# Kernel optimization log

Hardware: AMD Instinct MI355X
Metric: run time of the kernel (lower is better)

Reference implementation:

```python
import jax, jax.numpy as jnp
import numpy as np
from jax import lax

B, T, E, D = 32, 4096, 512, 512     # batch, x_steps, eunits, dunits
A, C, F = 128, 32, 15               # attn_dim, conv_channel, aconv_filts
K = 2 * F + 1                       # location conv kernel size
NEG = -1e9


def setup_inputs() -> dict:
    key = jax.random.key(0)
    ks = jax.random.split(key, 12)
    value = jax.random.normal(ks[0], (B, T, E), dtype=jnp.float32)
    value_length = jax.random.randint(ks[1], (B,), T // 2, T + 1).astype(jnp.int32)
    query = jax.random.normal(ks[2], (B, D), dtype=jnp.float32)
    # dirac initialization per initialize_weights()
    prev_attn_weight = jax.nn.one_hot(jnp.zeros((B,), jnp.int32), T, dtype=jnp.float32)
    accum_attn_weight = prev_attn_weight
    s = 0.02
    Wv = jax.random.normal(ks[3], (E, A), dtype=jnp.float32) * s
    bv = jnp.zeros((A,), jnp.float32)
    Wq = jax.random.normal(ks[4], (D, A), dtype=jnp.float32) * s
    conv_k = jax.random.normal(ks[5], (K, 1, C), dtype=jnp.float32) * s  # WIO
    Wl = jax.random.normal(ks[6], (C, A), dtype=jnp.float32) * s
    att_v = jax.random.normal(ks[7], (A,), dtype=jnp.float32)
    att_g = jnp.asarray(np.sqrt(1.0 / A), jnp.float32)
    att_b = jnp.zeros((A,), jnp.float32)
    score_bias = jnp.asarray(0.0, jnp.float32)
    return {"value": value, "value_length": value_length, "query": query,
            "accum_attn_weight": accum_attn_weight, "prev_attn_weight": prev_attn_weight,
            "Wv": Wv, "bv": bv, "Wq": Wq, "conv_k": conv_k, "Wl": Wl,
            "att_v": att_v, "att_g": att_g, "att_b": att_b, "score_bias": score_bias}


def _forward(value, value_length, query, accum_attn_weight, prev_attn_weight,
             Wv, bv, Wq, conv_k, Wl, att_v, att_g, att_b, score_bias):
    # projections
    densed_value = value @ Wv + bv                      # [B,T,A]
    densed_query = (query @ Wq)[:, None, :]             # [B,1,A]
    # location conv over accumulated weights, channels_last SAME
    loc = lax.conv_general_dilated(accum_attn_weight[:, :, None], conv_k,
                                   window_strides=(1,), padding='SAME',
                                   dimension_numbers=('NWC', 'WIO', 'NWC'))  # [B,T,C]
    attn_location = loc @ Wl                            # [B,T,A]
    # weight-normalized energy
    normed_v = att_g * att_v * lax.rsqrt(jnp.sum(jnp.square(att_v)))
    x = attn_location + densed_value + densed_query
    energy = jnp.einsum('bta,a->bt', jnp.tanh(x + att_b), normed_v) + score_bias
    mask = jnp.arange(T)[None, :] < value_length[:, None]
    energy = energy + (1.0 - mask.astype(energy.dtype)) * NEG
    # soft stepwise monotonic update (training=False: no sigmoid noise)
    p = jax.nn.sigmoid(energy)                          # [B,T]
    shifted = jnp.concatenate(
        [jnp.zeros((value.shape[0], 1), p.dtype),
         prev_attn_weight[:, :-1] * (1.0 - p[:, :-1])], axis=1)
    attn_weight = prev_attn_weight * p + shifted        # [B,T]
    attn_c = jnp.einsum('bt,bte->be', attn_weight, value)
    return attn_c, attn_weight


def reference(value, value_length, query, accum_attn_weight, prev_attn_weight,
              Wv, bv, Wq, conv_k, Wl, att_v, att_g, att_b, score_bias):
    return _forward(value, value_length, query, accum_attn_weight, prev_attn_weight,
                    Wv, bv, Wq, conv_k, Wl, att_v, att_g, att_b, score_bias)
```

## Files before the change

### kernel.cpp

```cpp
#include <hip/hip_runtime.h>
#include <hip/hip_bf16.h>

#define TT 4096
#define EE 512
#define AA 128

typedef short short8 __attribute__((ext_vector_type(8)));
typedef float f32x4 __attribute__((ext_vector_type(4)));

__device__ __forceinline__ short f2bf(float f) {
    union { float f; unsigned u; } v; v.f = f;
    unsigned r = v.u + 0x7fffu + ((v.u >> 16) & 1u);
    return (short)(r >> 16);
}

#define WS_WVT   0
#define WS_QBIAS 139264
#define WS_NV    155648
#define WS_P     156160
#define WS_PART  680448

__global__ void prep_wvt(const float* __restrict__ Wv, const float* __restrict__ conv_k,
                         const float* __restrict__ Wl, short* __restrict__ wvt) {
    int idx = blockIdx.x * 256 + threadIdx.x;
    int a = idx / 544, k = idx % 544;
    float val = 0.f;
    if (k < 512) {
        val = Wv[k * 128 + a];
    } else if (k < 543) {
        int kk = k - 512;
        float s = 0.f;
        #pragma unroll
        for (int c = 0; c < 32; ++c) s += conv_k[kk * 32 + c] * Wl[c * 128 + a];
        val = s;
    }
    wvt[a * 544 + k] = f2bf(val);
}

__global__ void prep_qbias(const float* __restrict__ query, const float* __restrict__ Wq,
                           const float* __restrict__ bv, const float* __restrict__ att_b,
                           const float* __restrict__ att_v, const float* __restrict__ att_g,
                           float* __restrict__ q_bias, float* __restrict__ nv) {
    int b = blockIdx.x, a = threadIdx.x;
    float s = 0.f;
    for (int d = 0; d < 512; ++d) s += query[b * 512 + d] * Wq[d * 128 + a];
    q_bias[b * 128 + a] = s + bv[a] + att_b[a];
    if (b == 0) {
        float ss = 0.f;
        for (int i = 0; i < 128; ++i) { float t = att_v[i]; ss += t * t; }
        nv[a] = att_g[0] * att_v[a] * rsqrtf(ss);
    }
}

__global__ __launch_bounds__(256) void energy_kernel(
    const float* __restrict__ value, const int* __restrict__ vlen,
    const float* __restrict__ accum, const short* __restrict__ wvt,
    const float* __restrict__ q_bias, const float* __restrict__ nv,
    const float* __restrict__ score_bias, float* __restrict__ p_buf) {

    __shared__ __align__(16) short As[64 * 40];
    __shared__ __align__(16) short Bs[128 * 40];

    int bid = blockIdx.x;
    int b  = bid >> 6;
    int t0 = (bid & 63) << 6;
    int tid = threadIdx.x;
    int l = tid & 63, w = tid >> 6;
    int l15 = l & 15, g = l >> 4;

    f32x4 acc[8];
    #pragma unroll
    for (int i = 0; i < 8; ++i) acc[i] = (f32x4){0.f, 0.f, 0.f, 0.f};

    int ar = tid >> 2;
    int ac = (tid & 3) * 8;
    int br = tid >> 1;
    int bc = (tid & 1) * 16;

    const float* aglob = value + ((size_t)(b * TT + t0 + ar)) * EE;

    for (int kc = 0; kc < 17; ++kc) {
        {
            const short* src = wvt + br * 544 + kc * 32 + bc;
            short8 s0 = *(const short8*)(src);
            short8 s1 = *(const short8*)(src + 8);
            *(short8*)(&Bs[br * 40 + bc])     = s0;
            *(short8*)(&Bs[br * 40 + bc + 8]) = s1;
        }
        if (kc < 16) {
            const float4* src = (const float4*)(aglob + kc * 32 + ac);
            float4 v0 = src[0], v1 = src[1];
            short8 h;
            h[0] = f2bf(v0.x); h[1] = f2bf(v0.y); h[2] = f2bf(v0.z); h[3] = f2bf(v0.w);
            h[4] = f2bf(v1.x); h[5] = f2bf(v1.y); h[6] = f2bf(v1.z); h[7] = f2bf(v1.w);
            *(short8*)(&As[ar * 40 + ac]) = h;
        } else {
            short8 h;
            #pragma unroll
            for (int i = 0; i < 8; ++i) {
                int kk = ac + i;
                int t = t0 + ar - 15 + kk;
                float v = (kk < 31 && t >= 0 && t < TT) ? accum[b * TT + t] : 0.f;
                h[i] = f2bf(v);
            }
            *(short8*)(&As[ar * 40 + ac]) = h;
        }
        __syncthreads();

        short8 af = *(const short8*)(&As[(w * 16 + l15) * 40 + g * 8]);
        #pragma unroll
        for (int t8 = 0; t8 < 8; ++t8) {
            short8 bf = *(const short8*)(&Bs[(t8 * 16 + l15) * 40 + g * 8]);
            acc[t8] = __builtin_amdgcn_mfma_f32_16x16x32_bf16(af, bf, acc[t8], 0, 0, 0);
        }
        __syncthreads();
    }

    float qb[8], nvv[8];
    #pragma unroll
    for (int t8 = 0; t8 < 8; ++t8) {
        int a = t8 * 16 + l15;
        qb[t8]  = q_bias[b * 128 + a];
        nvv[t8] = nv[a];
    }
    int len = vlen[b];
    float sb = score_bias[0];
    #pragma unroll
    for (int j = 0; j < 4; ++j) {
        float e = 0.f;
        #pragma unroll
        for (int t8 = 0; t8 < 8; ++t8)
            e += tanhf(acc[t8][j] + qb[t8]) * nvv[t8];
        e += __shfl_xor(e, 1);
        e += __shfl_xor(e, 2);
        e += __shfl_xor(e, 4);
        e += __shfl_xor(e, 8);
        if (l15 == 0) {
            int t = t0 + w * 16 + g * 4 + j;
            float p = 0.f;
            if (t < len) { float ee = e + sb; p = 1.f / (1.f + expf(-ee)); }
            p_buf[b * TT + t] = p;
        }
    }
}

__global__ void weight_kernel(const float* __restrict__ p_buf, const float* __restrict__ prev,
                              float* __restrict__ outw) {
    int i = blockIdx.x * 256 + threadIdx.x;
    int t = i & (TT - 1);
    float w = prev[i] * p_buf[i];
    if (t > 0) w += prev[i - 1] * (1.f - p_buf[i - 1]);
    outw[i] = w;
}

__global__ __launch_bounds__(256) void ctx_partial(const float* __restrict__ value,
                                                   const float* __restrict__ wbuf,
                                                   float* __restrict__ part) {
    __shared__ float wsm[512];
    int b = blockIdx.x, tc = blockIdx.y;
    int tid = threadIdx.x;
    wsm[tid]       = wbuf[b * TT + tc * 512 + tid];
    wsm[tid + 256] = wbuf[b * TT + tc * 512 + tid + 256];
    __syncthreads();
    float ax = 0.f, ay = 0.f;
    const float* vbase = value + ((size_t)b * TT + tc * 512) * EE + tid * 2;
    for (int tt = 0; tt < 512; ++tt) {
        float wv = wsm[tt];
        if (wv != 0.f) {
            float2 v = *(const float2*)(vbase + (size_t)tt * EE);
            ax += wv * v.x; ay += wv * v.y;
        }
    }
    float2 r; r.x = ax; r.y = ay;
    *(float2*)(part + ((b * 8 + tc) * 512) + tid * 2) = r;
}

__global__ void ctx_reduce(const float* __restrict__ part, float* __restrict__ outc) {
    int idx = blockIdx.x * 256 + threadIdx.x;
    int b = idx >> 9, e = idx & 511;
    float s = 0.f;
    #pragma unroll
    for (int tc = 0; tc < 8; ++tc) s += part[(b * 8 + tc) * 512 + e];
    outc[idx] = s;
}

extern "C" void kernel_launch(void* const* d_in, const int* in_sizes, int n_in,
                              void* d_out, int out_size, void* d_ws, size_t ws_size,
                              hipStream_t stream) {
    const float* value  = (const float*)d_in[0];
    const int*   vlen   = (const int*)  d_in[1];
    const float* query  = (const float*)d_in[2];
    const float* accum  = (const float*)d_in[3];
    const float* prev   = (const float*)d_in[4];
    const float* Wv     = (const float*)d_in[5];
    const float* bv     = (const float*)d_in[6];
    const float* Wq     = (const float*)d_in[7];
    const float* conv_k = (const float*)d_in[8];
    const float* Wl     = (const float*)d_in[9];
    const float* att_v  = (const float*)d_in[10];
    const float* att_g  = (const float*)d_in[11];
    const float* att_b  = (const float*)d_in[12];
    const float* sbias  = (const float*)d_in[13];

    char* wsb = (char*)d_ws;
    short* wvt   = (short*)(wsb + WS_WVT);
    float* qbias = (float*)(wsb + WS_QBIAS);
    float* nv    = (float*)(wsb + WS_NV);
    float* pbuf  = (float*)(wsb + WS_P);
    float* part  = (float*)(wsb + WS_PART);

    float* outc = (float*)d_out;
    float* outw = (float*)d_out + 32 * 512;

    prep_wvt   <<<272, 256, 0, stream>>>(Wv, conv_k, Wl, wvt);
    prep_qbias <<<32, 128, 0, stream>>>(query, Wq, bv, att_b, att_v, att_g, qbias, nv);
    energy_kernel<<<2048, 256, 0, stream>>>(value, vlen, accum, wvt, qbias, nv, sbias, pbuf);
    weight_kernel<<<512, 256, 0, stream>>>(pbuf, prev, outw);
    ctx_partial<<<dim3(32, 8), 256, 0, stream>>>(value, outw, part);
    ctx_reduce <<<64, 256, 0, stream>>>(part, outc);
}
```

Before: 465.5 us.

## Skip masked energy tiles, load MFMA operands directly from global, merge prep kernels

Energy blocks whose whole time tile lies beyond value_length now write zeros and exit, so value rows that the mask would discard are never read or multiplied. The shared-memory staging and barriers are gone: each lane loads its A fragment from value and its B fragment from the bf16 weight table straight into MFMA registers, relying on cache for weight reuse across waves. The two prep kernels are merged into one launch. Reuse through LDS is lost, so each wave re-reads the weights from L1/L2, and the uncoalesced per-lane row loads could cost more than the staging they replace.

```diff
diff --git a/kernel.cpp b/kernel.cpp
--- a/kernel.cpp
+++ b/kernel.cpp
@@ -20,35 +20,40 @@
 #define WS_P     156160
 #define WS_PART  680448
 
-__global__ void prep_wvt(const float* __restrict__ Wv, const float* __restrict__ conv_k,
-                         const float* __restrict__ Wl, short* __restrict__ wvt) {
-    int idx = blockIdx.x * 256 + threadIdx.x;
-    int a = idx / 544, k = idx % 544;
-    float val = 0.f;
-    if (k < 512) {
-        val = Wv[k * 128 + a];
-    } else if (k < 543) {
-        int kk = k - 512;
-        float s = 0.f;
-        #pragma unroll
-        for (int c = 0; c < 32; ++c) s += conv_k[kk * 32 + c] * Wl[c * 128 + a];
-        val = s;
-    }
-    wvt[a * 544 + k] = f2bf(val);
-}
-
-__global__ void prep_qbias(const float* __restrict__ query, const float* __restrict__ Wq,
-                           const float* __restrict__ bv, const float* __restrict__ att_b,
-                           const float* __restrict__ att_v, const float* __restrict__ att_g,
-                           float* __restrict__ q_bias, float* __restrict__ nv) {
-    int b = blockIdx.x, a = threadIdx.x;
-    float s = 0.f;
-    for (int d = 0; d < 512; ++d) s += query[b * 512 + d] * Wq[d * 128 + a];
-    q_bias[b * 128 + a] = s + bv[a] + att_b[a];
-    if (b == 0) {
-        float ss = 0.f;
-        for (int i = 0; i < 128; ++i) { float t = att_v[i]; ss += t * t; }
-        nv[a] = att_g[0] * att_v[a] * rsqrtf(ss);
+__global__ void prep_kernel(const float* __restrict__ Wv, const float* __restrict__ conv_k,
+                            const float* __restrict__ Wl, const float* __restrict__ query,
+                            const float* __restrict__ Wq, const float* __restrict__ bv,
+                            const float* __restrict__ att_b, const float* __restrict__ att_v,
+                            const float* __restrict__ att_g,
+                            short* __restrict__ wvt, float* __restrict__ q_bias,
+                            float* __restrict__ nv) {
+    if (blockIdx.x < 272) {
+        int idx = blockIdx.x * 256 + threadIdx.x;
+        int a = idx / 544, k = idx % 544;
+        float val = 0.f;
+        if (k < 512) {
+            val = Wv[k * 128 + a];
+        } else if (k < 543) {
+            int kk = k - 512;
+            float s = 0.f;
+            #pragma unroll
+            for (int c = 0; c < 32; ++c) s += conv_k[kk * 32 + c] * Wl[c * 128 + a];
+            val = s;
+        }
+        wvt[a * 544 + k] = f2bf(val);
+    } else {
+        int b = blockIdx.x - 272, a = threadIdx.x;
+        if (a < 128) {
+            float s = 0.f;
+            for (int d = 0; d < 512; ++d) s += query[b * 512 + d] * Wq[d * 128 + a];
+            q_bias[b * 128 + a] = s + bv[a] + att_b[a];
+            if (b == 0) {
+                float ss = 0.f;
+                #pragma unroll
+                for (int i = 0; i < 128; ++i) { float t = att_v[i]; ss += t * t; }
+                nv[a] = att_g[0] * att_v[a] * rsqrtf(ss);
+            }
+        }
     }
 }
 
@@ -58,62 +63,57 @@
     const float* __restrict__ q_bias, const float* __restrict__ nv,
     const float* __restrict__ score_bias, float* __restrict__ p_buf) {
 
-    __shared__ __align__(16) short As[64 * 40];
-    __shared__ __align__(16) short Bs[128 * 40];
-
     int bid = blockIdx.x;
     int b  = bid >> 6;
     int t0 = (bid & 63) << 6;
     int tid = threadIdx.x;
-    int l = tid & 63, w = tid >> 6;
+    int w = tid >> 6;
+    int l = tid & 63;
     int l15 = l & 15, g = l >> 4;
 
+    int len = vlen[b];
+    if (t0 >= len) {
+        if (tid < 64) p_buf[b * TT + t0 + tid] = 0.f;
+        return;
+    }
+
+    int row = t0 + w * 16 + l15;
+
     f32x4 acc[8];
     #pragma unroll
     for (int i = 0; i < 8; ++i) acc[i] = (f32x4){0.f, 0.f, 0.f, 0.f};
 
-    int ar = tid >> 2;
-    int ac = (tid & 3) * 8;
-    int br = tid >> 1;
-    int bc = (tid & 1) * 16;
-
-    const float* aglob = value + ((size_t)(b * TT + t0 + ar)) * EE;
-
-    for (int kc = 0; kc < 17; ++kc) {
-        {
-            const short* src = wvt + br * 544 + kc * 32 + bc;
-            short8 s0 = *(const short8*)(src);
-            short8 s1 = *(const short8*)(src + 8);
-            *(short8*)(&Bs[br * 40 + bc])     = s0;
-            *(short8*)(&Bs[br * 40 + bc + 8]) = s1;
-        }
-        if (kc < 16) {
-            const float4* src = (const float4*)(aglob + kc * 32 + ac);
-            float4 v0 = src[0], v1 = src[1];
-            short8 h;
-            h[0] = f2bf(v0.x); h[1] = f2bf(v0.y); h[2] = f2bf(v0.z); h[3] = f2bf(v0.w);
-            h[4] = f2bf(v1.x); h[5] = f2bf(v1.y); h[6] = f2bf(v1.z); h[7] = f2bf(v1.w);
-            *(short8*)(&As[ar * 40 + ac]) = h;
-        } else {
-            short8 h;
-            #pragma unroll
-            for (int i = 0; i < 8; ++i) {
-                int kk = ac + i;
-                int t = t0 + ar - 15 + kk;
-                float v = (kk < 31 && t >= 0 && t < TT) ? accum[b * TT + t] : 0.f;
-                h[i] = f2bf(v);
-            }
-            *(short8*)(&As[ar * 40 + ac]) = h;
-        }
-        __syncthreads();
-
-        short8 af = *(const short8*)(&As[(w * 16 + l15) * 40 + g * 8]);
+    const float* arow = value + ((size_t)(b * TT + row)) * EE + g * 8;
+    const short* brow = wvt + l15 * 544 + g * 8;
+
+    #pragma unroll 4
+    for (int kc = 0; kc < 16; ++kc) {
+        const float4* ap = (const float4*)(arow + kc * 32);
+        float4 v0 = ap[0], v1 = ap[1];
+        short8 af;
+        af[0] = f2bf(v0.x); af[1] = f2bf(v0.y); af[2] = f2bf(v0.z); af[3] = f2bf(v0.w);
+        af[4] = f2bf(v1.x); af[5] = f2bf(v1.y); af[6] = f2bf(v1.z); af[7] = f2bf(v1.w);
         #pragma unroll
         for (int t8 = 0; t8 < 8; ++t8) {
-            short8 bf = *(const short8*)(&Bs[(t8 * 16 + l15) * 40 + g * 8]);
+            short8 bf = *(const short8*)(brow + t8 * 16 * 544 + kc * 32);
             acc[t8] = __builtin_amdgcn_mfma_f32_16x16x32_bf16(af, bf, acc[t8], 0, 0, 0);
         }
-        __syncthreads();
+    }
+
+    {
+        short8 af;
+        #pragma unroll
+        for (int i = 0; i < 8; ++i) {
+            int kk = g * 8 + i;
+            int t = row - 15 + kk;
+            float v = (kk < 31 && t >= 0 && t < TT) ? accum[b * TT + t] : 0.f;
+            af[i] = f2bf(v);
+        }
+        #pragma unroll
+        for (int t8 = 0; t8 < 8; ++t8) {
+            short8 bf = *(const short8*)(brow + t8 * 16 * 544 + 512);
+            acc[t8] = __builtin_amdgcn_mfma_f32_16x16x32_bf16(af, bf, acc[t8], 0, 0, 0);
+        }
     }
 
     float qb[8], nvv[8];
@@ -123,7 +123,6 @@
         qb[t8]  = q_bias[b * 128 + a];
         nvv[t8] = nv[a];
     }
-    int len = vlen[b];
     float sb = score_bias[0];
     #pragma unroll
     for (int j = 0; j < 4; ++j) {
@@ -212,8 +211,8 @@
     float* outc = (float*)d_out;
     float* outw = (float*)d_out + 32 * 512;
 
-    prep_wvt   <<<272, 256, 0, stream>>>(Wv, conv_k, Wl, wvt);
-    prep_qbias <<<32, 128, 0, stream>>>(query, Wq, bv, att_b, att_v, att_g, qbias, nv);
+    prep_kernel<<<304, 256, 0, stream>>>(Wv, conv_k, Wl, query, Wq, bv, att_b,
+                                         att_v, att_g, wvt, qbias, nv);
     energy_kernel<<<2048, 256, 0, stream>>>(value, vlen, accum, wvt, qbias, nv, sbias, pbuf);
     weight_kernel<<<512, 256, 0, stream>>>(pbuf, prev, outw);
     ctx_partial<<<dim3(32, 8), 256, 0, stream>>>(value, outw, part);
```

Measured after the change: 503.8 us. 8.2% more time.
